# Kernel optimization log

Hardware: AMD Instinct MI355X
Metric: run time of the kernel (lower is better)

The kernel has to match this reference:

```python
import jax, jax.numpy as jnp
import numpy as np

N_NODES = 50000
N_EDGES = 800000
D_IN = 128
HIDDEN = 128
N_CLASSES = 40


def _sage_conv(x, edge_index, W_l, b_l, W_r, num_nodes):
    # PyG SAGEConv (aggr='mean'): out = lin_l(mean_j x_src_j) + lin_r(x_dst)
    src, dst = edge_index[0], edge_index[1]
    msg = x[src]                                              # [E, D] gather
    agg = jax.ops.segment_sum(msg, dst, num_segments=num_nodes)
    deg = jax.ops.segment_sum(jnp.ones((edge_index.shape[1],), x.dtype), dst,
                              num_segments=num_nodes)
    agg = agg / jnp.maximum(deg, 1.0)[:, None]                # scatter-mean
    return agg @ W_l + b_l + x @ W_r


def setup_inputs() -> dict:
    key = jax.random.key(0)
    k1, k2, k3, k4, k5, k6, k7 = jax.random.split(key, 7)
    s1 = 1.0 / np.sqrt(D_IN)
    s2 = 1.0 / np.sqrt(HIDDEN)
    return {
        "x": jax.random.normal(k1, (N_NODES, D_IN), dtype=jnp.float32),
        "edge_index": jax.random.randint(k2, (2, N_EDGES), 0, N_NODES, dtype=jnp.int64),
        "W1_l": jax.random.uniform(k3, (D_IN, HIDDEN), jnp.float32, -s1, s1),
        "b1": jnp.zeros((HIDDEN,), jnp.float32),
        "W1_r": jax.random.uniform(k4, (D_IN, HIDDEN), jnp.float32, -s1, s1),
        "W2_l": jax.random.uniform(k5, (HIDDEN, N_CLASSES), jnp.float32, -s2, s2),
        "b2": jnp.zeros((N_CLASSES,), jnp.float32),
        "W2_r": jax.random.uniform(k6, (HIDDEN, N_CLASSES), jnp.float32, -s2, s2),
    }


def reference(x, edge_index, W1_l, b1, W1_r, W2_l, b2, W2_r):
    # eval mode: F.dropout(training=False) is identity
    h = _sage_conv(x, edge_index, W1_l, b1, W1_r, N_NODES)
    h = jax.nn.relu(h)
    out = _sage_conv(h, edge_index, W2_l, b2, W2_r, N_NODES)
    return out
```

## Files before the change

### kernel.cpp

```cpp
#include <hip/hip_runtime.h>
#include <hip/hip_fp8.h>

#define N_NODES 50000
#define N_EDGES 800000
#define D_IN 128
#define HIDDEN 128
#define N_CLASSES 40

#define M_PAD 50048
#define CAP 64
#define EDGE_BATCH_BLOCKS 391
#define GEMM1_BLOCKS (M_PAD / 64)
#define FUSE_BLOCKS (EDGE_BATCH_BLOCKS + GEMM1_BLOCKS)

typedef __attribute__((ext_vector_type(8))) short short8;
typedef __attribute__((ext_vector_type(4))) float floatx4;

static __device__ __forceinline__ unsigned short f2bf(float f) {
    unsigned u = __float_as_uint(f);
    u = (u + 0x7fffu + ((u >> 16) & 1u)) >> 16;
    return (unsigned short)u;
}
static __device__ __forceinline__ float bf2f(unsigned short b) {
    return __uint_as_float(((unsigned)b) << 16);
}
static __device__ __forceinline__ unsigned char f2fp8(float v) {
    __hip_fp8_e4m3 t(v);
    return (unsigned char)t.__x;
}
static __device__ __forceinline__ float fp82f(unsigned char b) {
    __hip_fp8_e4m3 t;
    t.__x = (__hip_fp8_storage_t)b;
    return (float)t;
}

#define KP_W1 128
#define KP_W2 40
#define KP_CNT 196
#define KP_GRID (KP_W1 + KP_W2 + KP_CNT)

__global__ __launch_bounds__(256) void prep_kernel(
    const float* __restrict__ W1l, const float* __restrict__ W1r,
    unsigned short* __restrict__ Wt1, const float* __restrict__ W2l,
    const float* __restrict__ W2r, unsigned short* __restrict__ Wt2,
    int* __restrict__ cnt) {
    int b = blockIdx.x;
    int t = threadIdx.x;
    if (b < KP_W1) {
        int i = b * 256 + t;
        int n = i >> 7, k = i & 127;
        float v = (n < 128) ? W1l[k * 128 + n] : W1r[k * 128 + (n - 128)];
        Wt1[n * 128 + k] = f2bf(v);
    } else if (b < KP_W1 + KP_W2) {
        int i = (b - KP_W1) * 256 + t;
        int n = i >> 7, k = i & 127;
        float v = (n < 40) ? W2l[k * 40 + n] : W2r[k * 40 + (n - 40)];
        Wt2[n * 128 + k] = f2bf(v);
    } else {
        int i = (b - KP_W1 - KP_W2) * 256 + t;
        if (i < N_NODES) cnt[i] = 0;
    }
}

#define A_LD 136

__global__ __launch_bounds__(256) void fused_build_gemm1_kernel(
    const int* __restrict__ src, const int* __restrict__ dst,
    int* __restrict__ cnt, unsigned short* __restrict__ bucket,
    const float* __restrict__ x, const unsigned short* __restrict__ Wt,
    unsigned char* __restrict__ ylb, unsigned short* __restrict__ yrb) {
    __shared__ unsigned short sA[64][A_LD];

    if (blockIdx.x < EDGE_BATCH_BLOCKS) {
        int i0 = (blockIdx.x * 256 + threadIdx.x) * 8;
        if (i0 >= N_EDGES) return;
        int4 d0 = *(const int4*)(dst + i0);
        int4 d1 = *(const int4*)(dst + i0 + 4);
        int4 s0 = *(const int4*)(src + i0);
        int4 s1 = *(const int4*)(src + i0 + 4);
        int p0 = atomicAdd(&cnt[d0.x], 1);
        int p1 = atomicAdd(&cnt[d0.y], 1);
        int p2 = atomicAdd(&cnt[d0.z], 1);
        int p3 = atomicAdd(&cnt[d0.w], 1);
        int p4 = atomicAdd(&cnt[d1.x], 1);
        int p5 = atomicAdd(&cnt[d1.y], 1);
        int p6 = atomicAdd(&cnt[d1.z], 1);
        int p7 = atomicAdd(&cnt[d1.w], 1);
        if (p0 < CAP) bucket[d0.x * CAP + p0] = (unsigned short)s0.x;
        if (p1 < CAP) bucket[d0.y * CAP + p1] = (unsigned short)s0.y;
        if (p2 < CAP) bucket[d0.z * CAP + p2] = (unsigned short)s0.z;
        if (p3 < CAP) bucket[d0.w * CAP + p3] = (unsigned short)s0.w;
        if (p4 < CAP) bucket[d1.x * CAP + p4] = (unsigned short)s1.x;
        if (p5 < CAP) bucket[d1.y * CAP + p5] = (unsigned short)s1.y;
        if (p6 < CAP) bucket[d1.z * CAP + p6] = (unsigned short)s1.z;
        if (p7 < CAP) bucket[d1.w * CAP + p7] = (unsigned short)s1.w;
        return;
    }

    const int wave = threadIdx.x >> 6;
    const int lane = threadIdx.x & 63;
    const int r = lane & 15, q = lane >> 4;
    const int m0 = (blockIdx.x - EDGE_BATCH_BLOCKS) * 64;
    const int n0 = wave * 64;
    const int t = threadIdx.x;

#pragma unroll
    for (int i = 0; i < 8; i++) {
        int g = t + i * 256;
        int row = g >> 5;
        int k4 = (g & 31) << 2;
        int gr = m0 + row;
        if (gr >= N_NODES) gr = N_NODES - 1;
        float4 v = *(const float4*)(x + (size_t)gr * 128 + k4);
        uint2 p;
        p.x = (unsigned)f2bf(v.x) | ((unsigned)f2bf(v.y) << 16);
        p.y = (unsigned)f2bf(v.z) | ((unsigned)f2bf(v.w) << 16);
        *(uint2*)&sA[row][k4] = p;
    }
    __syncthreads();

    floatx4 acc[4][4];
#pragma unroll
    for (int i = 0; i < 4; i++)
#pragma unroll
        for (int j = 0; j < 4; j++) acc[i][j] = (floatx4){0.f, 0.f, 0.f, 0.f};

#pragma unroll
    for (int kc = 0; kc < 128; kc += 32) {
        short8 a[4], bb[4];
#pragma unroll
        for (int mi = 0; mi < 4; mi++)
            a[mi] = *(const short8*)&sA[mi * 16 + r][kc + q * 8];
#pragma unroll
        for (int ni = 0; ni < 4; ni++)
            bb[ni] = *(const short8*)(Wt + (size_t)(n0 + ni * 16 + r) * 128 + kc + q * 8);
#pragma unroll
        for (int mi = 0; mi < 4; mi++)
#pragma unroll
            for (int ni = 0; ni < 4; ni++)
                acc[mi][ni] = __builtin_amdgcn_mfma_f32_16x16x32_bf16(
                    a[mi], bb[ni], acc[mi][ni], 0, 0, 0);
    }

#pragma unroll
    for (int mi = 0; mi < 4; mi++) {
        int rowb = m0 + mi * 16 + q * 4;
#pragma unroll
        for (int ni = 0; ni < 4; ni++) {
            int col = n0 + ni * 16 + r;
#pragma unroll
            for (int reg = 0; reg < 4; reg++) {
                int gr = rowb + reg;
                if (gr < N_NODES) {
                    float v = acc[mi][ni][reg];
                    if (col < 128)
                        ylb[(size_t)gr * 128 + col] = f2fp8(v);
                    else
                        yrb[(size_t)gr * 128 + (col - 128)] = f2bf(v);
                }
            }
        }
    }
}

__global__ __launch_bounds__(256) void gemm2_mfma_kernel(
    const unsigned short* __restrict__ hb, const unsigned short* __restrict__ Wt,
    unsigned short* __restrict__ zlb, unsigned short* __restrict__ zrb) {
    const int wave = threadIdx.x >> 6;
    const int lane = threadIdx.x & 63;
    const int r = lane & 15, q = lane >> 4;
    const int m0 = blockIdx.x * 64 + wave * 16;

    floatx4 acc[5];
#pragma unroll
    for (int i = 0; i < 5; i++) acc[i] = (floatx4){0.f, 0.f, 0.f, 0.f};

#pragma unroll
    for (int kc = 0; kc < 128; kc += 32) {
        short8 a = *(const short8*)(hb + (size_t)(m0 + r) * 128 + kc + q * 8);
        short8 b[5];
#pragma unroll
        for (int ni = 0; ni < 5; ni++)
            b[ni] = *(const short8*)(Wt + (size_t)(ni * 16 + r) * 128 + kc + q * 8);
#pragma unroll
        for (int ni = 0; ni < 5; ni++)
            acc[ni] = __builtin_amdgcn_mfma_f32_16x16x32_bf16(a, b[ni], acc[ni], 0, 0, 0);
    }

    int rowb = m0 + q * 4;
#pragma unroll
    for (int ni = 0; ni < 5; ni++) {
        int col = ni * 16 + r;
#pragma unroll
        for (int reg = 0; reg < 4; reg++) {
            int gr = rowb + reg;
            if (gr < N_NODES) {
                unsigned short v = f2bf(acc[ni][reg]);
                if (col < 40)
                    zlb[(size_t)gr * 40 + col] = v;
                else
                    zrb[(size_t)gr * 40 + (col - 40)] = v;
            }
        }
    }
}

__global__ __launch_bounds__(256) void agg_relu1_kernel(
    const unsigned short* __restrict__ yl8, const int* __restrict__ cnt,
    const unsigned short* __restrict__ bucket, const float2* __restrict__ b12,
    const unsigned int* __restrict__ yru, unsigned int* __restrict__ hbu) {
    int n = blockIdx.x * 4 + (threadIdx.x >> 6);
    if (n >= N_NODES) return;
    int l = threadIdx.x & 63;
    int deg = cnt[n];
    int re = min(deg, CAP);
    const unsigned short* bk = bucket + n * CAP;
    float ax = 0.f, ay = 0.f, bx = 0.f, by = 0.f;
    int e = 0;
    for (; e + 7 < re; e += 8) {
        unsigned short u[8];
#pragma unroll
        for (int j = 0; j < 8; j++) {
            int s = bk[e + j];
            u[j] = yl8[(size_t)s * 64 + l];
        }
#pragma unroll
        for (int j = 0; j < 8; j += 2) {
            ax += fp82f(u[j] & 0xff); ay += fp82f(u[j] >> 8);
            bx += fp82f(u[j + 1] & 0xff); by += fp82f(u[j + 1] >> 8);
        }
    }
    for (; e + 3 < re; e += 4) {
        int s0 = bk[e + 0], s1 = bk[e + 1], s2 = bk[e + 2], s3 = bk[e + 3];
        unsigned short u0 = yl8[(size_t)s0 * 64 + l];
        unsigned short u1 = yl8[(size_t)s1 * 64 + l];
        unsigned short u2 = yl8[(size_t)s2 * 64 + l];
        unsigned short u3 = yl8[(size_t)s3 * 64 + l];
        ax += fp82f(u0 & 0xff); ay += fp82f(u0 >> 8);
        bx += fp82f(u1 & 0xff); by += fp82f(u1 >> 8);
        ax += fp82f(u2 & 0xff); ay += fp82f(u2 >> 8);
        bx += fp82f(u3 & 0xff); by += fp82f(u3 >> 8);
    }
    for (; e < re; e++) {
        unsigned short u0 = yl8[(size_t)bk[e] * 64 + l];
        ax += fp82f(u0 & 0xff); ay += fp82f(u0 >> 8);
    }
    float inv = 1.0f / (float)max(deg, 1);
    unsigned ur = yru[(size_t)n * 64 + l];
    float2 b = b12[l];
    float ox = fmaxf((ax + bx) * inv + bf2f(ur & 0xffff) + b.x, 0.0f);
    float oy = fmaxf((ay + by) * inv + bf2f(ur >> 16) + b.y, 0.0f);
    hbu[(size_t)n * 64 + l] = (unsigned)f2bf(ox) | ((unsigned)f2bf(oy) << 16);
}

__global__ __launch_bounds__(256) void agg_out2_kernel(
    const unsigned short* __restrict__ zlb, const unsigned short* __restrict__ zrb,
    const int* __restrict__ cnt, const unsigned short* __restrict__ bucket,
    const float* __restrict__ b2, float* __restrict__ out) {
    int n = blockIdx.x * 4 + (threadIdx.x >> 6);
    if (n >= N_NODES) return;
    int c = threadIdx.x & 63;
    if (c >= N_CLASSES) return;
    int deg = cnt[n];
    int re = min(deg, CAP);
    const unsigned short* bk = bucket + n * CAP;
    float a0 = 0.f, a1 = 0.f;
    int e = 0;
    for (; e + 3 < re; e += 4) {
        int s0 = bk[e + 0], s1 = bk[e + 1], s2 = bk[e + 2], s3 = bk[e + 3];
        float v0 = bf2f(zlb[(size_t)s0 * 40 + c]);
        float v1 = bf2f(zlb[(size_t)s1 * 40 + c]);
        float v2 = bf2f(zlb[(size_t)s2 * 40 + c]);
        float v3 = bf2f(zlb[(size_t)s3 * 40 + c]);
        a0 += v0 + v2;
        a1 += v1 + v3;
    }
    for (; e < re; e++) a0 += bf2f(zlb[(size_t)bk[e] * 40 + c]);
    float inv = 1.0f / (float)max(deg, 1);
    out[(size_t)n * 40 + c] =
        (a0 + a1) * inv + bf2f(zrb[(size_t)n * 40 + c]) + b2[c];
}

extern "C" void kernel_launch(void* const* d_in, const int* in_sizes, int n_in,
                              void* d_out, int out_size, void* d_ws, size_t ws_size,
                              hipStream_t stream) {
    const float* x   = (const float*)d_in[0];
    const int*   ei  = (const int*)d_in[1];
    const float* W1l = (const float*)d_in[2];
    const float* b1  = (const float*)d_in[3];
    const float* W1r = (const float*)d_in[4];
    const float* W2l = (const float*)d_in[5];
    const float* b2  = (const float*)d_in[6];
    const float* W2r = (const float*)d_in[7];
    float* out = (float*)d_out;

    const int* src = ei;
    const int* dst = ei + N_EDGES;

    char* ws = (char*)d_ws;
    int* cnt               = (int*)(ws);
    unsigned short* bucket = (unsigned short*)(ws + 262144);
    unsigned short* Wt1    = (unsigned short*)(ws + 6662144);
    unsigned short* Wt2    = (unsigned short*)(ws + 6727680);
    unsigned short* hb     = (unsigned short*)(ws + 6748160);
    unsigned char*  ylb    = (unsigned char*)(ws + 19560448);
    unsigned short* yrb    = (unsigned short*)(ws + 25960448);
    unsigned short* zlb    = (unsigned short*)(ws + 38760448);
    unsigned short* zrb    = (unsigned short*)(ws + 42760448);

    prep_kernel<<<KP_GRID, 256, 0, stream>>>(W1l, W1r, Wt1, W2l, W2r, Wt2, cnt);

    fused_build_gemm1_kernel<<<FUSE_BLOCKS, 256, 0, stream>>>(
        src, dst, cnt, bucket, x, Wt1, ylb, yrb);

    const int AGG_BLOCKS = (N_NODES + 3) / 4;

    agg_relu1_kernel<<<AGG_BLOCKS, 256, 0, stream>>>(
        (const unsigned short*)ylb, cnt, bucket, (const float2*)b1,
        (const unsigned int*)yrb, (unsigned int*)hb);

    gemm2_mfma_kernel<<<M_PAD / 64, 256, 0, stream>>>(hb, Wt2, zlb, zrb);
    agg_out2_kernel<<<AGG_BLOCKS, 256, 0, stream>>>(
        zlb, zrb, cnt, bucket, b2, out);
}
```

Baseline: 212.1 us.

## Fuse layer-1 aggregation+ReLU into GEMM2 via shared-memory hidden tile

Merges the layer-1 mean aggregation, bias and ReLU kernel with the second GEMM. Each block aggregates 64 nodes (16 per wave, processed serially), writes the bf16 hidden rows into LDS, then runs the MFMA GEMM straight from LDS. This removes one launch and the global write and read of the hidden activation buffer. In exchange the grid shrinks from about 12.5k blocks to 782, and each wave handles its nodes one after another, which cuts latency hiding for the gather-bound aggregation.

```diff
diff --git a/kernel.cpp b/kernel.cpp
--- a/kernel.cpp
+++ b/kernel.cpp
@@ -163,13 +163,66 @@
     }
 }
 
-__global__ __launch_bounds__(256) void gemm2_mfma_kernel(
-    const unsigned short* __restrict__ hb, const unsigned short* __restrict__ Wt,
+__global__ __launch_bounds__(256) void agg_gemm2_kernel(
+    const unsigned short* __restrict__ yl8, const int* __restrict__ cnt,
+    const unsigned short* __restrict__ bucket, const float2* __restrict__ b12,
+    const unsigned int* __restrict__ yru, const unsigned short* __restrict__ Wt,
     unsigned short* __restrict__ zlb, unsigned short* __restrict__ zrb) {
+    __shared__ unsigned short sH[64][A_LD];
+
     const int wave = threadIdx.x >> 6;
-    const int lane = threadIdx.x & 63;
-    const int r = lane & 15, q = lane >> 4;
-    const int m0 = blockIdx.x * 64 + wave * 16;
+    const int l = threadIdx.x & 63;
+    const int nodeBase = blockIdx.x * 64;
+
+    for (int nd = 0; nd < 16; nd++) {
+        const int lrow = wave * 16 + nd;
+        int n = nodeBase + lrow;
+        if (n >= N_NODES) n = N_NODES - 1;
+        int deg = cnt[n];
+        int re = min(deg, CAP);
+        const unsigned short* bk = bucket + n * CAP;
+        float ax = 0.f, ay = 0.f, bx = 0.f, by = 0.f;
+        int e = 0;
+        for (; e + 7 < re; e += 8) {
+            unsigned short u[8];
+#pragma unroll
+            for (int j = 0; j < 8; j++) {
+                int s = bk[e + j];
+                u[j] = yl8[(size_t)s * 64 + l];
+            }
+#pragma unroll
+            for (int j = 0; j < 8; j += 2) {
+                ax += fp82f(u[j] & 0xff); ay += fp82f(u[j] >> 8);
+                bx += fp82f(u[j + 1] & 0xff); by += fp82f(u[j + 1] >> 8);
+            }
+        }
+        for (; e + 3 < re; e += 4) {
+            int s0 = bk[e + 0], s1 = bk[e + 1], s2 = bk[e + 2], s3 = bk[e + 3];
+            unsigned short u0 = yl8[(size_t)s0 * 64 + l];
+            unsigned short u1 = yl8[(size_t)s1 * 64 + l];
+            unsigned short u2 = yl8[(size_t)s2 * 64 + l];
+            unsigned short u3 = yl8[(size_t)s3 * 64 + l];
+            ax += fp82f(u0 & 0xff); ay += fp82f(u0 >> 8);
+            bx += fp82f(u1 & 0xff); by += fp82f(u1 >> 8);
+            ax += fp82f(u2 & 0xff); ay += fp82f(u2 >> 8);
+            bx += fp82f(u3 & 0xff); by += fp82f(u3 >> 8);
+        }
+        for (; e < re; e++) {
+            unsigned short u0 = yl8[(size_t)bk[e] * 64 + l];
+            ax += fp82f(u0 & 0xff); ay += fp82f(u0 >> 8);
+        }
+        float inv = 1.0f / (float)max(deg, 1);
+        unsigned ur = yru[(size_t)n * 64 + l];
+        float2 b = b12[l];
+        float ox = fmaxf((ax + bx) * inv + bf2f(ur & 0xffff) + b.x, 0.0f);
+        float oy = fmaxf((ay + by) * inv + bf2f(ur >> 16) + b.y, 0.0f);
+        *(unsigned*)&sH[lrow][2 * l] =
+            (unsigned)f2bf(ox) | ((unsigned)f2bf(oy) << 16);
+    }
+    __syncthreads();
+
+    const int r = l & 15, q = l >> 4;
+    const int m0 = nodeBase + wave * 16;
 
     floatx4 acc[5];
 #pragma unroll
@@ -177,7 +230,7 @@
 
 #pragma unroll
     for (int kc = 0; kc < 128; kc += 32) {
-        short8 a = *(const short8*)(hb + (size_t)(m0 + r) * 128 + kc + q * 8);
+        short8 a = *(const short8*)&sH[wave * 16 + r][kc + q * 8];
         short8 b[5];
 #pragma unroll
         for (int ni = 0; ni < 5; ni++)
@@ -203,54 +256,6 @@
             }
         }
     }
-}
-
-__global__ __launch_bounds__(256) void agg_relu1_kernel(
-    const unsigned short* __restrict__ yl8, const int* __restrict__ cnt,
-    const unsigned short* __restrict__ bucket, const float2* __restrict__ b12,
-    const unsigned int* __restrict__ yru, unsigned int* __restrict__ hbu) {
-    int n = blockIdx.x * 4 + (threadIdx.x >> 6);
-    if (n >= N_NODES) return;
-    int l = threadIdx.x & 63;
-    int deg = cnt[n];
-    int re = min(deg, CAP);
-    const unsigned short* bk = bucket + n * CAP;
-    float ax = 0.f, ay = 0.f, bx = 0.f, by = 0.f;
-    int e = 0;
-    for (; e + 7 < re; e += 8) {
-        unsigned short u[8];
-#pragma unroll
-        for (int j = 0; j < 8; j++) {
-            int s = bk[e + j];
-            u[j] = yl8[(size_t)s * 64 + l];
-        }
-#pragma unroll
-        for (int j = 0; j < 8; j += 2) {
-            ax += fp82f(u[j] & 0xff); ay += fp82f(u[j] >> 8);
-            bx += fp82f(u[j + 1] & 0xff); by += fp82f(u[j + 1] >> 8);
-        }
-    }
-    for (; e + 3 < re; e += 4) {
-        int s0 = bk[e + 0], s1 = bk[e + 1], s2 = bk[e + 2], s3 = bk[e + 3];
-        unsigned short u0 = yl8[(size_t)s0 * 64 + l];
-        unsigned short u1 = yl8[(size_t)s1 * 64 + l];
-        unsigned short u2 = yl8[(size_t)s2 * 64 + l];
-        unsigned short u3 = yl8[(size_t)s3 * 64 + l];
-        ax += fp82f(u0 & 0xff); ay += fp82f(u0 >> 8);
-        bx += fp82f(u1 & 0xff); by += fp82f(u1 >> 8);
-        ax += fp82f(u2 & 0xff); ay += fp82f(u2 >> 8);
-        bx += fp82f(u3 & 0xff); by += fp82f(u3 >> 8);
-    }
-    for (; e < re; e++) {
-        unsigned short u0 = yl8[(size_t)bk[e] * 64 + l];
-        ax += fp82f(u0 & 0xff); ay += fp82f(u0 >> 8);
-    }
-    float inv = 1.0f / (float)max(deg, 1);
-    unsigned ur = yru[(size_t)n * 64 + l];
-    float2 b = b12[l];
-    float ox = fmaxf((ax + bx) * inv + bf2f(ur & 0xffff) + b.x, 0.0f);
-    float oy = fmaxf((ay + by) * inv + bf2f(ur >> 16) + b.y, 0.0f);
-    hbu[(size_t)n * 64 + l] = (unsigned)f2bf(ox) | ((unsigned)f2bf(oy) << 16);
 }
 
 __global__ __launch_bounds__(256) void agg_out2_kernel(
@@ -302,7 +307,6 @@
     unsigned short* bucket = (unsigned short*)(ws + 262144);
     unsigned short* Wt1    = (unsigned short*)(ws + 6662144);
     unsigned short* Wt2    = (unsigned short*)(ws + 6727680);
-    unsigned short* hb     = (unsigned short*)(ws + 6748160);
     unsigned char*  ylb    = (unsigned char*)(ws + 19560448);
     unsigned short* yrb    = (unsigned short*)(ws + 25960448);
     unsigned short* zlb    = (unsigned short*)(ws + 38760448);
@@ -313,13 +317,11 @@
     fused_build_gemm1_kernel<<<FUSE_BLOCKS, 256, 0, stream>>>(
         src, dst, cnt, bucket, x, Wt1, ylb, yrb);
 
+    agg_gemm2_kernel<<<GEMM1_BLOCKS, 256, 0, stream>>>(
+        (const unsigned short*)ylb, cnt, bucket, (const float2*)b1,
+        (const unsigned int*)yrb, Wt2, zlb, zrb);
+
     const int AGG_BLOCKS = (N_NODES + 3) / 4;
-
-    agg_relu1_kernel<<<AGG_BLOCKS, 256, 0, stream>>>(
-        (const unsigned short*)ylb, cnt, bucket, (const float2*)b1,
-        (const unsigned int*)yrb, (unsigned int*)hb);
-
-    gemm2_mfma_kernel<<<M_PAD / 64, 256, 0, stream>>>(hb, Wt2, zlb, zrb);
     agg_out2_kernel<<<AGG_BLOCKS, 256, 0, stream>>>(
         zlb, zrb, cnt, bucket, b2, out);
 }
```

Result: slower. 227.8 us (+7.4%).
